# Optimization experiments

Hardware: AMD Instinct MI355X
Metric: run time of the kernel (lower is better)

Reference implementation:

```python
import jax, jax.numpy as jnp
import numpy as np

N = 50000      # nodes
E = 800000     # edges
IN_DIM = 512
OUT_DIM = 64
NUM_HEADS = 8
NEG_SLOPE = 0.2


def setup_inputs() -> dict:
    key = jax.random.key(0)
    ks = jax.random.split(key, 8)
    feat = jax.random.normal(ks[0], (N, IN_DIM), dtype=jnp.float32)
    dist = jax.random.uniform(ks[1], (E, NUM_HEADS), dtype=jnp.float32)
    src = jax.random.randint(ks[2], (E,), 0, N, dtype=jnp.int32)
    dst = jax.random.randint(ks[3], (E,), 0, N, dtype=jnp.int32)
    # learned parameters (match torch init scales loosely)
    W = jax.random.normal(ks[4], (NUM_HEADS * OUT_DIM, IN_DIM), dtype=jnp.float32) / np.sqrt(IN_DIM)
    b = jax.random.normal(ks[5], (NUM_HEADS * OUT_DIM,), dtype=jnp.float32) * 0.01
    w_att_src = jax.random.normal(ks[6], (NUM_HEADS, OUT_DIM), dtype=jnp.float32)
    w_att_dst = jax.random.normal(ks[7], (NUM_HEADS, OUT_DIM), dtype=jnp.float32)
    return {"feat": feat, "dist": dist, "src": src, "dst": dst,
            "W": W, "b": b, "w_att_src": w_att_src, "w_att_dst": w_att_dst}


def reference(feat, dist, src, dst, W, b, w_att_src, w_att_dst):
    # Linear + LeakyReLU: [N, H*D]
    h = jax.nn.leaky_relu(feat @ W.T + b, negative_slope=NEG_SLOPE)
    h = h.reshape(N, NUM_HEADS, OUT_DIM)          # [N, H, D]
    # per-node attention logits
    e_src = jnp.sum(h * w_att_src, axis=-1)        # [N, H]
    e_dst = jnp.sum(h * w_att_dst, axis=-1)        # [N, H]
    # gather onto edges (u_add_v) + LeakyReLU
    e = jax.nn.leaky_relu(e_src[src] + e_dst[dst], negative_slope=NEG_SLOPE)  # [E, H]
    # edge_softmax: segment softmax over incoming edges of each dst node
    m = jax.ops.segment_max(e, dst, num_segments=N)      # [N, H]
    ex = jnp.exp(e - m[dst])                             # [E, H]
    s = jax.ops.segment_sum(ex, dst, num_segments=N)     # [N, H]
    a = (ex / s[dst]) * dist                             # [E, H]
    # u_mul_e + sum aggregation
    msg = h[src] * a[:, :, None]                         # [E, H, D]
    out = jax.ops.segment_sum(msg, dst, num_segments=N)  # [N, H, D]
    return out.reshape(N, NUM_HEADS * OUT_DIM)
```

## Files before the change

### kernel.cpp

```cpp
#include <hip/hip_runtime.h>

#define NNODES 50000
#define NEDGES 800000
#define INDIM  512
#define OUTD   512
#define NHEADS 8

typedef float  f32x4  __attribute__((ext_vector_type(4)));
typedef __bf16 bf16x8 __attribute__((ext_vector_type(8)));
typedef __bf16 bf16x4 __attribute__((ext_vector_type(4)));

__device__ __forceinline__ float lrelu(float x) { return x > 0.f ? x : 0.2f * x; }

constexpr int BM = 128, BN = 128, BK = 32, LDA = BK + 8;

__global__ __launch_bounds__(256) void gemm_h(
    const float* __restrict__ feat, const float* __restrict__ W,
    const float* __restrict__ bias, const float* __restrict__ w_s,
    const float* __restrict__ w_d, __bf16* __restrict__ hout,
    float* __restrict__ esrc, float* __restrict__ edst)
{
    __shared__ __bf16 As[BM][LDA];
    __shared__ __bf16 Bs[BN][LDA];
    const int row0 = blockIdx.x * BM;
    const int col0 = blockIdx.y * BN;
    const int tid  = threadIdx.x;
    const int lane = tid & 63;
    const int w    = tid >> 6;
    const int wr   = w >> 1, wc = w & 1;
    const int lr   = lane & 15, kg = lane >> 4;

    f32x4 acc[4][4] = {};

    for (int k0 = 0; k0 < INDIM; k0 += BK) {
        #pragma unroll
        for (int i = 0; i < 4; ++i) {
            int idx = tid + 256 * i;
            int r = idx >> 3, c4 = idx & 7;
            int gr = row0 + r;
            f32x4 v = {0.f, 0.f, 0.f, 0.f};
            if (gr < NNODES) v = *(const f32x4*)(feat + (size_t)gr * INDIM + k0 + c4 * 4);
            bf16x4 bv; bv[0]=(__bf16)v[0]; bv[1]=(__bf16)v[1]; bv[2]=(__bf16)v[2]; bv[3]=(__bf16)v[3];
            *(bf16x4*)&As[r][c4 * 4] = bv;
            f32x4 u = *(const f32x4*)(W + (size_t)(col0 + r) * INDIM + k0 + c4 * 4);
            bf16x4 bu; bu[0]=(__bf16)u[0]; bu[1]=(__bf16)u[1]; bu[2]=(__bf16)u[2]; bu[3]=(__bf16)u[3];
            *(bf16x4*)&Bs[r][c4 * 4] = bu;
        }
        __syncthreads();
        bf16x8 af[4], bf[4];
        #pragma unroll
        for (int mi = 0; mi < 4; ++mi) af[mi] = *(const bf16x8*)&As[wr * 64 + mi * 16 + lr][kg * 8];
        #pragma unroll
        for (int ni = 0; ni < 4; ++ni) bf[ni] = *(const bf16x8*)&Bs[wc * 64 + ni * 16 + lr][kg * 8];
        #pragma unroll
        for (int mi = 0; mi < 4; ++mi)
            #pragma unroll
            for (int ni = 0; ni < 4; ++ni)
                acc[mi][ni] = __builtin_amdgcn_mfma_f32_16x16x32_bf16(af[mi], bf[ni], acc[mi][ni], 0, 0, 0);
        __syncthreads();
    }

    float cb[4], wsv[4], wdv[4];
    #pragma unroll
    for (int ni = 0; ni < 4; ++ni) {
        int c = col0 + wc * 64 + ni * 16 + lr;
        cb[ni]  = bias[c];
        wsv[ni] = w_s[c];
        wdv[ni] = w_d[c];
    }
    const int head = (col0 + wc * 64) >> 6;
    #pragma unroll
    for (int mi = 0; mi < 4; ++mi) {
        #pragma unroll
        for (int reg = 0; reg < 4; ++reg) {
            int r = row0 + wr * 64 + mi * 16 + kg * 4 + reg;
            bool valid = r < NNODES;
            float vs = 0.f, vd = 0.f;
            #pragma unroll
            for (int ni = 0; ni < 4; ++ni) {
                int c = col0 + wc * 64 + ni * 16 + lr;
                float v = acc[mi][ni][reg] + cb[ni];
                v = lrelu(v);
                if (valid) hout[(size_t)r * OUTD + c] = (__bf16)v;
                vs += v * wsv[ni];
                vd += v * wdv[ni];
            }
            #pragma unroll
            for (int m = 1; m < 16; m <<= 1) { vs += __shfl_xor(vs, m); vd += __shfl_xor(vd, m); }
            if (valid && lr == 0) {
                esrc[r * NHEADS + head] = vs;
                edst[r * NHEADS + head] = vd;
            }
        }
    }
}

__global__ void hist_k(const int* __restrict__ dstv, int* __restrict__ deg)
{
    int e = blockIdx.x * blockDim.x + threadIdx.x;
    if (e < NEDGES) atomicAdd(&deg[dstv[e]], 1);
}

__global__ __launch_bounds__(256) void scan_bsums(const int* __restrict__ deg, int* __restrict__ bsums)
{
    __shared__ int sd[256];
    int t = threadIdx.x, base = blockIdx.x * 1024, sum = 0;
    #pragma unroll
    for (int i = 0; i < 4; ++i) { int idx = base + t * 4 + i; if (idx < NNODES) sum += deg[idx]; }
    sd[t] = sum; __syncthreads();
    for (int st = 128; st > 0; st >>= 1) { if (t < st) sd[t] += sd[t + st]; __syncthreads(); }
    if (t == 0) bsums[blockIdx.x] = sd[0];
}

__global__ void scan_partials(int* __restrict__ bsums)
{
    int l = threadIdx.x;
    int orig = (l < 49) ? bsums[l] : 0;
    int v = orig;
    #pragma unroll
    for (int d = 1; d < 64; d <<= 1) { int u = __shfl_up(v, d); if (l >= d) v += u; }
    if (l < 49) bsums[l] = v - orig;
}

__global__ __launch_bounds__(256) void scan_final(
    const int* __restrict__ deg, const int* __restrict__ bsums, int* __restrict__ offs)
{
    __shared__ int sd[256];
    int t = threadIdx.x, base = blockIdx.x * 1024;
    int v[4]; int sum = 0;
    #pragma unroll
    for (int i = 0; i < 4; ++i) { int idx = base + t * 4 + i; v[i] = (idx < NNODES) ? deg[idx] : 0; sum += v[i]; }
    sd[t] = sum; __syncthreads();
    int val = sum;
    for (int st = 1; st < 256; st <<= 1) {
        int add = (t >= st) ? sd[t - st] : 0;
        __syncthreads();
        val += add; sd[t] = val;
        __syncthreads();
    }
    int run = bsums[blockIdx.x] + (val - sum);
    #pragma unroll
    for (int i = 0; i < 4; ++i) { int idx = base + t * 4 + i; if (idx < NNODES) offs[idx] = run; run += v[i]; }
    if (blockIdx.x == 0 && t == 0) offs[NNODES] = NEDGES;
}

__global__ void scatter_k(const int* __restrict__ dstv, int* __restrict__ cursor, int* __restrict__ eidx)
{
    int e = blockIdx.x * blockDim.x + threadIdx.x;
    if (e < NEDGES) { int pos = atomicAdd(&cursor[dstv[e]], 1); eidx[pos] = e; }
}

__global__ __launch_bounds__(256) void agg_k(
    const int* __restrict__ offs, const int* __restrict__ eidx,
    const int* __restrict__ src, const float* __restrict__ esrc,
    const float* __restrict__ edst, const float* __restrict__ dist,
    const __bf16* __restrict__ hmat, float* __restrict__ out)
{
    int node = blockIdx.x * 4 + (threadIdx.x >> 6);
    int lane = threadIdx.x & 63;
    if (node >= NNODES) return;
    const int head = lane >> 3;
    const float edv = edst[(size_t)node * NHEADS + head];
    int beg = offs[node], end = offs[node + 1];
    float denom = 0.f;
    float acc[8] = {0.f, 0.f, 0.f, 0.f, 0.f, 0.f, 0.f, 0.f};

    if (beg < end) {
        int e  = eidx[beg];
        int sn = src[e];
        for (int pos = beg; pos < end; ++pos) {
            int e_cur = e, sn_cur = sn;
            if (pos + 1 < end) {
                e  = eidx[pos + 1];
                sn = src[e];
            }
            float ex = __expf(lrelu(esrc[(size_t)sn_cur * NHEADS + head] + edv));
            float a  = ex * dist[(size_t)e_cur * NHEADS + head];
            denom += ex;
            bf16x8 hv = *(const bf16x8*)(hmat + (size_t)sn_cur * OUTD + lane * 8);
            #pragma unroll
            for (int j = 0; j < 8; ++j) acc[j] += a * (float)hv[j];
        }
    }

    float sinv = denom > 0.f ? 1.f / denom : 0.f;
    f32x4 o0 = {acc[0] * sinv, acc[1] * sinv, acc[2] * sinv, acc[3] * sinv};
    f32x4 o1 = {acc[4] * sinv, acc[5] * sinv, acc[6] * sinv, acc[7] * sinv};
    *(f32x4*)(out + (size_t)node * OUTD + lane * 8)     = o0;
    *(f32x4*)(out + (size_t)node * OUTD + lane * 8 + 4) = o1;
}

extern "C" void kernel_launch(void* const* d_in, const int* in_sizes, int n_in,
                              void* d_out, int out_size, void* d_ws, size_t ws_size,
                              hipStream_t stream)
{
    const float* feat = (const float*)d_in[0];
    const float* dist = (const float*)d_in[1];
    const int*   src  = (const int*)d_in[2];
    const int*   dstv = (const int*)d_in[3];
    const float* W    = (const float*)d_in[4];
    const float* bias = (const float*)d_in[5];
    const float* w_s  = (const float*)d_in[6];
    const float* w_d  = (const float*)d_in[7];
    float* out = (float*)d_out;

    char* wsb = (char*)d_ws;
    size_t off = 0;
    auto alloc = [&](size_t bytes) -> char* {
        char* r = wsb + off;
        off = (off + bytes + 255) & ~(size_t)255;
        return r;
    };
    __bf16* hmat  = (__bf16*)alloc((size_t)NNODES * OUTD * 2);
    float*  esrc  = (float*)alloc((size_t)NNODES * NHEADS * 4);
    float*  edst  = (float*)alloc((size_t)NNODES * NHEADS * 4);
    int*    deg   = (int*)alloc((size_t)NNODES * 4);
    int*    offs  = (int*)alloc((size_t)(NNODES + 1) * 4);
    int*    cursor= (int*)alloc((size_t)NNODES * 4);
    int*    eidx  = (int*)alloc((size_t)NEDGES * 4);
    int*    bsums = (int*)alloc(64 * 4);

    hipMemsetAsync(deg, 0, (size_t)NNODES * 4, stream);

    gemm_h<<<dim3((NNODES + BM - 1) / BM, OUTD / BN), 256, 0, stream>>>(
        feat, W, bias, w_s, w_d, hmat, esrc, edst);

    hist_k<<<(NEDGES + 255) / 256, 256, 0, stream>>>(dstv, deg);
    scan_bsums<<<49, 256, 0, stream>>>(deg, bsums);
    scan_partials<<<1, 64, 0, stream>>>(bsums);
    scan_final<<<49, 256, 0, stream>>>(deg, bsums, offs);
    hipMemcpyAsync(cursor, offs, (size_t)NNODES * 4, hipMemcpyDeviceToDevice, stream);
    scatter_k<<<(NEDGES + 255) / 256, 256, 0, stream>>>(dstv, cursor, eidx);

    agg_k<<<(NNODES + 3) / 4, 256, 0, stream>>>(offs, eidx, src, esrc, edst, dist, hmat, out);
}
```

Before: 554.6 us.

## Fuse degree histogram into GEMM, pack src with edge id, unroll aggregation

The degree histogram now runs inside the GEMM kernel, each block handling 512 edges, which removes a separate launch. scan_final writes the cursor copy directly, so the device-to-device memcpy goes away. The scatter step stores (src, edge id) pairs, so aggregation no longer does a dependent src lookup per edge. The aggregation loop is unrolled by 4 to keep more independent gathers in flight. In exchange the permutation buffer is twice as large and the GEMM blocks do extra atomic work.

```diff
diff --git a/kernel.cpp b/kernel.cpp
--- a/kernel.cpp
+++ b/kernel.cpp
@@ -18,13 +18,23 @@
     const float* __restrict__ feat, const float* __restrict__ W,
     const float* __restrict__ bias, const float* __restrict__ w_s,
     const float* __restrict__ w_d, __bf16* __restrict__ hout,
-    float* __restrict__ esrc, float* __restrict__ edst)
+    float* __restrict__ esrc, float* __restrict__ edst,
+    const int* __restrict__ dstv, int* __restrict__ deg)
 {
     __shared__ __bf16 As[BM][LDA];
     __shared__ __bf16 Bs[BN][LDA];
     const int row0 = blockIdx.x * BM;
     const int col0 = blockIdx.y * BN;
     const int tid  = threadIdx.x;
+
+    {
+        int bid = blockIdx.y * gridDim.x + blockIdx.x;
+        int lo = bid * 512, hi = lo + 512;
+        if (hi > NEDGES) hi = NEDGES;
+        for (int e = lo + tid; e < hi; e += 256)
+            atomicAdd(&deg[dstv[e]], 1);
+    }
+
     const int lane = tid & 63;
     const int w    = tid >> 6;
     const int wr   = w >> 1, wc = w & 1;
@@ -95,12 +105,6 @@
     }
 }
 
-__global__ void hist_k(const int* __restrict__ dstv, int* __restrict__ deg)
-{
-    int e = blockIdx.x * blockDim.x + threadIdx.x;
-    if (e < NEDGES) atomicAdd(&deg[dstv[e]], 1);
-}
-
 __global__ __launch_bounds__(256) void scan_bsums(const int* __restrict__ deg, int* __restrict__ bsums)
 {
     __shared__ int sd[256];
@@ -123,7 +127,8 @@
 }
 
 __global__ __launch_bounds__(256) void scan_final(
-    const int* __restrict__ deg, const int* __restrict__ bsums, int* __restrict__ offs)
+    const int* __restrict__ deg, const int* __restrict__ bsums,
+    int* __restrict__ offs, int* __restrict__ cursor)
 {
     __shared__ int sd[256];
     int t = threadIdx.x, base = blockIdx.x * 1024;
@@ -140,21 +145,29 @@
     }
     int run = bsums[blockIdx.x] + (val - sum);
     #pragma unroll
-    for (int i = 0; i < 4; ++i) { int idx = base + t * 4 + i; if (idx < NNODES) offs[idx] = run; run += v[i]; }
+    for (int i = 0; i < 4; ++i) {
+        int idx = base + t * 4 + i;
+        if (idx < NNODES) { offs[idx] = run; cursor[idx] = run; }
+        run += v[i];
+    }
     if (blockIdx.x == 0 && t == 0) offs[NNODES] = NEDGES;
 }
 
-__global__ void scatter_k(const int* __restrict__ dstv, int* __restrict__ cursor, int* __restrict__ eidx)
+__global__ void scatter_k(const int* __restrict__ dstv, const int* __restrict__ src,
+                          int* __restrict__ cursor, int2* __restrict__ perm)
 {
     int e = blockIdx.x * blockDim.x + threadIdx.x;
-    if (e < NEDGES) { int pos = atomicAdd(&cursor[dstv[e]], 1); eidx[pos] = e; }
+    if (e < NEDGES) {
+        int pos = atomicAdd(&cursor[dstv[e]], 1);
+        perm[pos] = make_int2(src[e], e);
+    }
 }
 
 __global__ __launch_bounds__(256) void agg_k(
-    const int* __restrict__ offs, const int* __restrict__ eidx,
-    const int* __restrict__ src, const float* __restrict__ esrc,
-    const float* __restrict__ edst, const float* __restrict__ dist,
-    const __bf16* __restrict__ hmat, float* __restrict__ out)
+    const int* __restrict__ offs, const int2* __restrict__ perm,
+    const float* __restrict__ esrc, const float* __restrict__ edst,
+    const float* __restrict__ dist, const __bf16* __restrict__ hmat,
+    float* __restrict__ out)
 {
     int node = blockIdx.x * 4 + (threadIdx.x >> 6);
     int lane = threadIdx.x & 63;
@@ -163,24 +176,44 @@
     const float edv = edst[(size_t)node * NHEADS + head];
     int beg = offs[node], end = offs[node + 1];
     float denom = 0.f;
-    float acc[8] = {0.f, 0.f, 0.f, 0.f, 0.f, 0.f, 0.f, 0.f};
-
-    if (beg < end) {
-        int e  = eidx[beg];
-        int sn = src[e];
-        for (int pos = beg; pos < end; ++pos) {
-            int e_cur = e, sn_cur = sn;
-            if (pos + 1 < end) {
-                e  = eidx[pos + 1];
-                sn = src[e];
-            }
-            float ex = __expf(lrelu(esrc[(size_t)sn_cur * NHEADS + head] + edv));
-            float a  = ex * dist[(size_t)e_cur * NHEADS + head];
-            denom += ex;
-            bf16x8 hv = *(const bf16x8*)(hmat + (size_t)sn_cur * OUTD + lane * 8);
-            #pragma unroll
-            for (int j = 0; j < 8; ++j) acc[j] += a * (float)hv[j];
-        }
+    float acc[8] = {};
+
+    int pos = beg;
+    for (; pos + 4 <= end; pos += 4) {
+        int2 a0 = perm[pos], a1 = perm[pos + 1], a2 = perm[pos + 2], a3 = perm[pos + 3];
+        float es0 = esrc[(size_t)a0.x * NHEADS + head];
+        float es1 = esrc[(size_t)a1.x * NHEADS + head];
+        float es2 = esrc[(size_t)a2.x * NHEADS + head];
+        float es3 = esrc[(size_t)a3.x * NHEADS + head];
+        float di0 = dist[(size_t)a0.y * NHEADS + head];
+        float di1 = dist[(size_t)a1.y * NHEADS + head];
+        float di2 = dist[(size_t)a2.y * NHEADS + head];
+        float di3 = dist[(size_t)a3.y * NHEADS + head];
+        bf16x8 h0 = *(const bf16x8*)(hmat + (size_t)a0.x * OUTD + lane * 8);
+        bf16x8 h1 = *(const bf16x8*)(hmat + (size_t)a1.x * OUTD + lane * 8);
+        bf16x8 h2 = *(const bf16x8*)(hmat + (size_t)a2.x * OUTD + lane * 8);
+        bf16x8 h3 = *(const bf16x8*)(hmat + (size_t)a3.x * OUTD + lane * 8);
+        float ex0 = __expf(lrelu(es0 + edv));
+        float ex1 = __expf(lrelu(es1 + edv));
+        float ex2 = __expf(lrelu(es2 + edv));
+        float ex3 = __expf(lrelu(es3 + edv));
+        denom += (ex0 + ex1) + (ex2 + ex3);
+        float w0 = ex0 * di0, w1 = ex1 * di1, w2 = ex2 * di2, w3 = ex3 * di3;
+        #pragma unroll
+        for (int j = 0; j < 8; ++j)
+            acc[j] += (w0 * (float)h0[j] + w1 * (float)h1[j])
+                    + (w2 * (float)h2[j] + w3 * (float)h3[j]);
+    }
+    for (; pos < end; ++pos) {
+        int2 a0 = perm[pos];
+        float es0 = esrc[(size_t)a0.x * NHEADS + head];
+        float di0 = dist[(size_t)a0.y * NHEADS + head];
+        bf16x8 h0 = *(const bf16x8*)(hmat + (size_t)a0.x * OUTD + lane * 8);
+        float ex0 = __expf(lrelu(es0 + edv));
+        denom += ex0;
+        float w0 = ex0 * di0;
+        #pragma unroll
+        for (int j = 0; j < 8; ++j) acc[j] += w0 * (float)h0[j];
     }
 
     float sinv = denom > 0.f ? 1.f / denom : 0.f;
@@ -217,20 +250,18 @@
     int*    deg   = (int*)alloc((size_t)NNODES * 4);
     int*    offs  = (int*)alloc((size_t)(NNODES + 1) * 4);
     int*    cursor= (int*)alloc((size_t)NNODES * 4);
-    int*    eidx  = (int*)alloc((size_t)NEDGES * 4);
+    int2*   perm  = (int2*)alloc((size_t)NEDGES * 8);
     int*    bsums = (int*)alloc(64 * 4);
 
     hipMemsetAsync(deg, 0, (size_t)NNODES * 4, stream);
 
     gemm_h<<<dim3((NNODES + BM - 1) / BM, OUTD / BN), 256, 0, stream>>>(
-        feat, W, bias, w_s, w_d, hmat, esrc, edst);
-
-    hist_k<<<(NEDGES + 255) / 256, 256, 0, stream>>>(dstv, deg);
+        feat, W, bias, w_s, w_d, hmat, esrc, edst, dstv, deg);
+
     scan_bsums<<<49, 256, 0, stream>>>(deg, bsums);
     scan_partials<<<1, 64, 0, stream>>>(bsums);
-    scan_final<<<49, 256, 0, stream>>>(deg, bsums, offs);
-    hipMemcpyAsync(cursor, offs, (size_t)NNODES * 4, hipMemcpyDeviceToDevice, stream);
-    scatter_k<<<(NEDGES + 255) / 256, 256, 0, stream>>>(dstv, cursor, eidx);
-
-    agg_k<<<(NNODES + 3) / 4, 256, 0, stream>>>(offs, eidx, src, esrc, edst, dist, hmat, out);
-}
+    scan_final<<<49, 256, 0, stream>>>(deg, bsums, offs, cursor);
+    scatter_k<<<(NEDGES + 255) / 256, 256, 0, stream>>>(dstv, src, cursor, perm);
+
+    agg_k<<<(NNODES + 3) / 4, 256, 0, stream>>>(offs, perm, esrc, edst, dist, hmat, out);
+}
```

After: 524.3 us. -5.4%, faster.
